# Kernel tuning notes

Measured on AMD Instinct MI355X. Metric: run time of the kernel, lower is better.

## Reference

```python
import jax, jax.numpy as jnp
import numpy as np
from jax import lax

V, E, H, S, B = 32000, 150, 30, 128, 32
STDV = 1.0 / np.sqrt(30.0)


def setup_inputs() -> dict:
    key = jax.random.key(0)
    ks = jax.random.split(key, 9)
    u = lambda k, shape: jax.random.uniform(k, shape, jnp.float32, -STDV, STDV)
    return {
        "input_batch": jax.random.randint(ks[0], (S, B), 0, V),
        "embedding": u(ks[1], (V, E)),
        "W_ih_lr": u(ks[2], (E + H, H)),
        "b_ih_lr": u(ks[3], (1, H)),
        "W_ih_rl": u(ks[4], (E + H, H)),
        "b_ih_rl": u(ks[5], (1, H)),
        "W_ho": u(ks[6], (2 * H, V)),
        "b_ho": u(ks[7], (1, V)),
        "initial_hidden": u(ks[8], (1, H)),
    }


def reference(input_batch, embedding, W_ih_lr, b_ih_lr, W_ih_rl, b_ih_rl,
              W_ho, b_ho, initial_hidden):
    seq_len, batch = input_batch.shape
    emb = embedding[input_batch]  # (S, B, E)
    # original code detaches the initial hidden state (uses .data)
    init = jnp.broadcast_to(lax.stop_gradient(initial_hidden), (batch, initial_hidden.shape[1]))

    def step(W, b):
        def f(h, w):
            h_new = jnp.tanh(jnp.concatenate([w, h], axis=1) @ W + b)
            return h_new, h_new
        return f

    # forward (left-to-right): f_states[t] = hLR[t+1]
    _, f_states = lax.scan(step(W_ih_lr, b_ih_lr), init, emb)
    # backward (right-to-left) over reversed tokens: r_states[k] = hRL[S-1-k]
    _, r_states = lax.scan(step(W_ih_rl, b_ih_rl), init, emb[::-1])

    # prediction at i uses hLR[i] and hRL[i+1]
    hLR_used = jnp.concatenate([init[None], f_states[:-1]], axis=0)        # hLR[0..S-1]
    hRL_used = jnp.concatenate([r_states[:-1][::-1], init[None]], axis=0)  # hRL[1..S]

    h_cat = jnp.concatenate([hLR_used, hRL_used], axis=-1)  # (S, B, 2H)
    logits = jnp.einsum('sbh,hv->sbv', h_cat, W_ho) + b_ho  # (S, B, V)
    return jax.nn.log_softmax(logits, axis=-1)
```

## Files before the change

kernel.cpp:

```cpp
#include <hip/hip_runtime.h>

#define VSZ 32000
#define ESZ 150
#define HSZ 30
#define SSZ 128
#define BSZ 32
#define SB  4096
#define KP  64

typedef __attribute__((ext_vector_type(8))) short bf16x8;
typedef __attribute__((ext_vector_type(4))) float f32x4;
typedef __attribute__((ext_vector_type(8))) unsigned short u16x8;

static __device__ __forceinline__ unsigned short f2bf(float f) {
  unsigned int u = __float_as_uint(f);
  u += 0x7fffu + ((u >> 16) & 1u);
  return (unsigned short)(u >> 16);
}

__global__ void k_zproj(const int* __restrict__ idx, const float* __restrict__ emb,
                        const float* __restrict__ Wlr, const float* __restrict__ blr,
                        const float* __restrict__ Wrl, const float* __restrict__ brl,
                        float* __restrict__ z) {
  __shared__ float erow[ESZ];
  int tb = blockIdx.x;
  int row = idx[tb];
  for (int i = threadIdx.x; i < ESZ; i += 64) erow[i] = emb[row * ESZ + i];
  __syncthreads();
  int lane = threadIdx.x;
  int j = lane & 31, dir = lane >> 5;
  if (j < HSZ) {
    const float* W = dir ? Wrl : Wlr;
    float acc = dir ? brl[j] : blr[j];
#pragma unroll 10
    for (int e = 0; e < ESZ; ++e) acc = fmaf(erow[e], W[e * HSZ + j], acc);
    z[(dir * SB + tb) * HSZ + j] = acc;
  }
}

__global__ void k_scan(const float* __restrict__ z, const float* __restrict__ Wlr,
                       const float* __restrict__ Wrl, const float* __restrict__ h0,
                       unsigned short* __restrict__ hcat) {
  int lane = threadIdx.x;
  int half = lane >> 5, j = lane & 31;
  int chain = blockIdx.x * 2 + half;
  int dir = chain >> 5, b = chain & 31;
  const float* W = dir ? Wrl : Wlr;
  float w2[HSZ];
#pragma unroll
  for (int k = 0; k < HSZ; ++k) w2[k] = (j < HSZ) ? W[(ESZ + k) * HSZ + j] : 0.f;
  float h = (j < HSZ) ? h0[j] : 0.f;
  int dim = (j < HSZ) ? dir * HSZ + j : (dir ? 60 : 62) + (j - 30);
  unsigned short padbits = (dim == 60) ? f2bf(1.0f) : (unsigned short)0;
  const float* zc = z + dir * (SB * HSZ) + b * HSZ + j;
  int src = half << 5;
  int te0 = dir ? (SSZ - 1) : 0;
  float zv = (j < HSZ) ? zc[te0 * (BSZ * HSZ)] : 0.f;
  for (int t = 0; t < SSZ; ++t) {
    int te = dir ? (SSZ - 1 - t) : t;
    float zn = 0.f;
    if (t < SSZ - 1) {
      int ten = dir ? (SSZ - 2 - t) : (t + 1);
      zn = (j < HSZ) ? zc[ten * (BSZ * HSZ)] : 0.f;
    }
    int r = te * BSZ + b;
    hcat[r * KP + dim] = (j < HSZ) ? f2bf(h) : padbits;
    float a0 = zv, a1 = 0.f, a2 = 0.f, a3 = 0.f;
#pragma unroll
    for (int k = 0; k < 28; k += 4) {
      a0 = fmaf(__shfl(h, src + k),     w2[k],     a0);
      a1 = fmaf(__shfl(h, src + k + 1), w2[k + 1], a1);
      a2 = fmaf(__shfl(h, src + k + 2), w2[k + 2], a2);
      a3 = fmaf(__shfl(h, src + k + 3), w2[k + 3], a3);
    }
    a0 = fmaf(__shfl(h, src + 28), w2[28], a0);
    a1 = fmaf(__shfl(h, src + 29), w2[29], a1);
    float x = (a0 + a1) + (a2 + a3);
    h = tanhf(x);
    zv = zn;
  }
}

__global__ void k_wprep(const float* __restrict__ Who, const float* __restrict__ bho,
                        unsigned short* __restrict__ Wbt) {
  int v = blockIdx.x * 256 + threadIdx.x;
  int kq = blockIdx.y;
  u16x8 pack;
#pragma unroll
  for (int i = 0; i < 8; ++i) {
    int k = kq * 8 + i;
    float val = (k < 60) ? Who[k * VSZ + v] : ((k == 60) ? bho[v] : 0.f);
    pack[i] = f2bf(val);
  }
  *(u16x8*)&Wbt[v * KP + kq * 8] = pack;
}

__global__ void k_sumexp(const unsigned short* __restrict__ hcat,
                         const unsigned short* __restrict__ Wbt,
                         float* __restrict__ part) {
  int mb = blockIdx.x, nb = blockIdx.y;
  int wave = threadIdx.x >> 6, lane = threadIdx.x & 63;
  int g = lane >> 4, c = lane & 15;
  int rbase = mb * 128 + wave * 32;
  bf16x8 a[2][2];
#pragma unroll
  for (int mt = 0; mt < 2; ++mt)
#pragma unroll
    for (int ks = 0; ks < 2; ++ks)
      a[mt][ks] = *(const bf16x8*)&hcat[(rbase + mt * 16 + c) * KP + ks * 32 + g * 8];
  float se[2][4] = {{0.f, 0.f, 0.f, 0.f}, {0.f, 0.f, 0.f, 0.f}};
  int c0 = nb * 2000;
  for (int nt = 0; nt < 125; ++nt) {
    int col = c0 + nt * 16 + c;
    bf16x8 b0 = *(const bf16x8*)&Wbt[col * KP + g * 8];
    bf16x8 b1 = *(const bf16x8*)&Wbt[col * KP + 32 + g * 8];
#pragma unroll
    for (int mt = 0; mt < 2; ++mt) {
      f32x4 acc = {0.f, 0.f, 0.f, 0.f};
      acc = __builtin_amdgcn_mfma_f32_16x16x32_bf16(a[mt][0], b0, acc, 0, 0, 0);
      acc = __builtin_amdgcn_mfma_f32_16x16x32_bf16(a[mt][1], b1, acc, 0, 0, 0);
#pragma unroll
      for (int i = 0; i < 4; ++i) se[mt][i] += __expf(acc[i]);
    }
  }
#pragma unroll
  for (int off = 1; off < 16; off <<= 1)
#pragma unroll
    for (int mt = 0; mt < 2; ++mt)
#pragma unroll
      for (int i = 0; i < 4; ++i) se[mt][i] += __shfl_xor(se[mt][i], off);
  if (c == 0) {
#pragma unroll
    for (int mt = 0; mt < 2; ++mt)
#pragma unroll
      for (int i = 0; i < 4; ++i)
        part[(rbase + mt * 16 + g * 4 + i) * 16 + nb] = se[mt][i];
  }
}

__global__ void k_writeout(const unsigned short* __restrict__ hcat,
                           const unsigned short* __restrict__ Wbt,
                           const float* __restrict__ part,
                           float* __restrict__ out) {
  __shared__ float Lsh[128];
  int mb = blockIdx.x, nb = blockIdx.y;
  int tid = threadIdx.x;
  if (tid < 128) {
    const float* p = &part[(mb * 128 + tid) * 16];
    float s = 0.f;
#pragma unroll
    for (int k = 0; k < 16; ++k) s += p[k];
    Lsh[tid] = logf(s);
  }
  __syncthreads();
  int wave = tid >> 6, lane = tid & 63;
  int g = lane >> 4, c = lane & 15;
  int rbase = mb * 128 + wave * 32;
  bf16x8 a[2][2];
#pragma unroll
  for (int mt = 0; mt < 2; ++mt)
#pragma unroll
    for (int ks = 0; ks < 2; ++ks)
      a[mt][ks] = *(const bf16x8*)&hcat[(rbase + mt * 16 + c) * KP + ks * 32 + g * 8];
  float L[2][4];
#pragma unroll
  for (int mt = 0; mt < 2; ++mt)
#pragma unroll
    for (int i = 0; i < 4; ++i)
      L[mt][i] = Lsh[wave * 32 + mt * 16 + g * 4 + i];
  int c0 = nb * 2000;
  for (int nt = 0; nt < 125; ++nt) {
    int col = c0 + nt * 16 + c;
    bf16x8 b0 = *(const bf16x8*)&Wbt[col * KP + g * 8];
    bf16x8 b1 = *(const bf16x8*)&Wbt[col * KP + 32 + g * 8];
#pragma unroll
    for (int mt = 0; mt < 2; ++mt) {
      f32x4 acc = {0.f, 0.f, 0.f, 0.f};
      acc = __builtin_amdgcn_mfma_f32_16x16x32_bf16(a[mt][0], b0, acc, 0, 0, 0);
      acc = __builtin_amdgcn_mfma_f32_16x16x32_bf16(a[mt][1], b1, acc, 0, 0, 0);
#pragma unroll
      for (int i = 0; i < 4; ++i)
        out[(rbase + mt * 16 + g * 4 + i) * VSZ + col] = acc[i] - L[mt][i];
    }
  }
}

extern "C" void kernel_launch(void* const* d_in, const int* in_sizes, int n_in,
                              void* d_out, int out_size, void* d_ws, size_t ws_size,
                              hipStream_t stream) {
  (void)in_sizes; (void)n_in; (void)out_size; (void)ws_size;
  const int*   idx = (const int*)d_in[0];
  const float* emb = (const float*)d_in[1];
  const float* Wlr = (const float*)d_in[2];
  const float* blr = (const float*)d_in[3];
  const float* Wrl = (const float*)d_in[4];
  const float* brl = (const float*)d_in[5];
  const float* Who = (const float*)d_in[6];
  const float* bho = (const float*)d_in[7];
  const float* h0  = (const float*)d_in[8];
  float* out = (float*)d_out;

  char* ws = (char*)d_ws;
  float*          z    = (float*)(ws + 0);
  unsigned short* hcat = (unsigned short*)(ws + 983040);
  unsigned short* Wbt  = (unsigned short*)(ws + 1507328);
  float*          part = (float*)(ws + 5603328);

  k_zproj<<<SB, 64, 0, stream>>>(idx, emb, Wlr, blr, Wrl, brl, z);
  k_wprep<<<dim3(125, 8), 256, 0, stream>>>(Who, bho, Wbt);
  k_scan<<<32, 64, 0, stream>>>(z, Wlr, Wrl, h0, hcat);
  k_sumexp<<<dim3(32, 16), 256, 0, stream>>>(hcat, Wbt, part);
  k_writeout<<<dim3(32, 16), 256, 0, stream>>>(hcat, Wbt, part, out);
}
```

Measured before the change: 321.1 us.

## Swap MFMA operands for row-contiguous vector stores, readlane scan, fast tanh

The output GEMMs now put the weight tile in the A operand and the hidden states in B. Each lane therefore holds four consecutive vocab columns of one row, so the log-softmax output can be written with 16-byte vector stores instead of scattered scalar stores, and the sum-exp reduction gets simpler. The recurrent scan now runs one chain per 64-lane block and broadcasts hidden values with readlane instead of shuffles. It also replaces tanhf with an exp-based formula, which may lose a little accuracy near zero. The launch order of the scan and the weight-prep kernel is swapped.

```diff
diff --git a/kernel.cpp b/kernel.cpp
--- a/kernel.cpp
+++ b/kernel.cpp
@@ -16,6 +16,10 @@
   unsigned int u = __float_as_uint(f);
   u += 0x7fffu + ((u >> 16) & 1u);
   return (unsigned short)(u >> 16);
+}
+
+static __device__ __forceinline__ float readlane_f(float v, int lane) {
+  return __uint_as_float(__builtin_amdgcn_readlane(__float_as_uint(v), lane));
 }
 
 __global__ void k_zproj(const int* __restrict__ idx, const float* __restrict__ emb,
@@ -41,19 +45,18 @@
 __global__ void k_scan(const float* __restrict__ z, const float* __restrict__ Wlr,
                        const float* __restrict__ Wrl, const float* __restrict__ h0,
                        unsigned short* __restrict__ hcat) {
-  int lane = threadIdx.x;
-  int half = lane >> 5, j = lane & 31;
-  int chain = blockIdx.x * 2 + half;
+  int j = threadIdx.x;
+  int chain = blockIdx.x;
   int dir = chain >> 5, b = chain & 31;
   const float* W = dir ? Wrl : Wlr;
   float w2[HSZ];
 #pragma unroll
   for (int k = 0; k < HSZ; ++k) w2[k] = (j < HSZ) ? W[(ESZ + k) * HSZ + j] : 0.f;
   float h = (j < HSZ) ? h0[j] : 0.f;
+  bool wr = (j < 32);
   int dim = (j < HSZ) ? dir * HSZ + j : (dir ? 60 : 62) + (j - 30);
   unsigned short padbits = (dim == 60) ? f2bf(1.0f) : (unsigned short)0;
   const float* zc = z + dir * (SB * HSZ) + b * HSZ + j;
-  int src = half << 5;
   int te0 = dir ? (SSZ - 1) : 0;
   float zv = (j < HSZ) ? zc[te0 * (BSZ * HSZ)] : 0.f;
   for (int t = 0; t < SSZ; ++t) {
@@ -64,19 +67,20 @@
       zn = (j < HSZ) ? zc[ten * (BSZ * HSZ)] : 0.f;
     }
     int r = te * BSZ + b;
-    hcat[r * KP + dim] = (j < HSZ) ? f2bf(h) : padbits;
+    if (wr) hcat[r * KP + dim] = (j < HSZ) ? f2bf(h) : padbits;
     float a0 = zv, a1 = 0.f, a2 = 0.f, a3 = 0.f;
 #pragma unroll
     for (int k = 0; k < 28; k += 4) {
-      a0 = fmaf(__shfl(h, src + k),     w2[k],     a0);
-      a1 = fmaf(__shfl(h, src + k + 1), w2[k + 1], a1);
-      a2 = fmaf(__shfl(h, src + k + 2), w2[k + 2], a2);
-      a3 = fmaf(__shfl(h, src + k + 3), w2[k + 3], a3);
-    }
-    a0 = fmaf(__shfl(h, src + 28), w2[28], a0);
-    a1 = fmaf(__shfl(h, src + 29), w2[29], a1);
+      a0 = fmaf(readlane_f(h, k),     w2[k],     a0);
+      a1 = fmaf(readlane_f(h, k + 1), w2[k + 1], a1);
+      a2 = fmaf(readlane_f(h, k + 2), w2[k + 2], a2);
+      a3 = fmaf(readlane_f(h, k + 3), w2[k + 3], a3);
+    }
+    a0 = fmaf(readlane_f(h, 28), w2[28], a0);
+    a1 = fmaf(readlane_f(h, 29), w2[29], a1);
     float x = (a0 + a1) + (a2 + a3);
-    h = tanhf(x);
+    float e = __expf(2.0f * x);
+    h = 1.0f - __fdividef(2.0f, e + 1.0f);
     zv = zn;
   }
 }
@@ -102,39 +106,35 @@
   int wave = threadIdx.x >> 6, lane = threadIdx.x & 63;
   int g = lane >> 4, c = lane & 15;
   int rbase = mb * 128 + wave * 32;
-  bf16x8 a[2][2];
-#pragma unroll
-  for (int mt = 0; mt < 2; ++mt)
+  bf16x8 bfr[2][2];
+#pragma unroll
+  for (int rg = 0; rg < 2; ++rg)
 #pragma unroll
     for (int ks = 0; ks < 2; ++ks)
-      a[mt][ks] = *(const bf16x8*)&hcat[(rbase + mt * 16 + c) * KP + ks * 32 + g * 8];
-  float se[2][4] = {{0.f, 0.f, 0.f, 0.f}, {0.f, 0.f, 0.f, 0.f}};
+      bfr[rg][ks] = *(const bf16x8*)&hcat[(rbase + rg * 16 + c) * KP + ks * 32 + g * 8];
+  float se[2] = {0.f, 0.f};
   int c0 = nb * 2000;
   for (int nt = 0; nt < 125; ++nt) {
-    int col = c0 + nt * 16 + c;
-    bf16x8 b0 = *(const bf16x8*)&Wbt[col * KP + g * 8];
-    bf16x8 b1 = *(const bf16x8*)&Wbt[col * KP + 32 + g * 8];
-#pragma unroll
-    for (int mt = 0; mt < 2; ++mt) {
+    int ct = c0 + nt * 16;
+    bf16x8 a0 = *(const bf16x8*)&Wbt[(ct + c) * KP + g * 8];
+    bf16x8 a1 = *(const bf16x8*)&Wbt[(ct + c) * KP + 32 + g * 8];
+#pragma unroll
+    for (int rg = 0; rg < 2; ++rg) {
       f32x4 acc = {0.f, 0.f, 0.f, 0.f};
-      acc = __builtin_amdgcn_mfma_f32_16x16x32_bf16(a[mt][0], b0, acc, 0, 0, 0);
-      acc = __builtin_amdgcn_mfma_f32_16x16x32_bf16(a[mt][1], b1, acc, 0, 0, 0);
-#pragma unroll
-      for (int i = 0; i < 4; ++i) se[mt][i] += __expf(acc[i]);
-    }
-  }
-#pragma unroll
-  for (int off = 1; off < 16; off <<= 1)
-#pragma unroll
-    for (int mt = 0; mt < 2; ++mt)
-#pragma unroll
-      for (int i = 0; i < 4; ++i) se[mt][i] += __shfl_xor(se[mt][i], off);
-  if (c == 0) {
-#pragma unroll
-    for (int mt = 0; mt < 2; ++mt)
-#pragma unroll
-      for (int i = 0; i < 4; ++i)
-        part[(rbase + mt * 16 + g * 4 + i) * 16 + nb] = se[mt][i];
+      acc = __builtin_amdgcn_mfma_f32_16x16x32_bf16(a0, bfr[rg][0], acc, 0, 0, 0);
+      acc = __builtin_amdgcn_mfma_f32_16x16x32_bf16(a1, bfr[rg][1], acc, 0, 0, 0);
+      se[rg] += (__expf(acc[0]) + __expf(acc[1])) + (__expf(acc[2]) + __expf(acc[3]));
+    }
+  }
+#pragma unroll
+  for (int rg = 0; rg < 2; ++rg) {
+    se[rg] += __shfl_xor(se[rg], 16);
+    se[rg] += __shfl_xor(se[rg], 32);
+  }
+  if (g == 0) {
+#pragma unroll
+    for (int rg = 0; rg < 2; ++rg)
+      part[(rbase + rg * 16 + c) * 16 + nb] = se[rg];
   }
 }
 
@@ -156,31 +156,29 @@
   int wave = tid >> 6, lane = tid & 63;
   int g = lane >> 4, c = lane & 15;
   int rbase = mb * 128 + wave * 32;
-  bf16x8 a[2][2];
-#pragma unroll
-  for (int mt = 0; mt < 2; ++mt)
+  bf16x8 bfr[2][2];
+#pragma unroll
+  for (int rg = 0; rg < 2; ++rg)
 #pragma unroll
     for (int ks = 0; ks < 2; ++ks)
-      a[mt][ks] = *(const bf16x8*)&hcat[(rbase + mt * 16 + c) * KP + ks * 32 + g * 8];
-  float L[2][4];
-#pragma unroll
-  for (int mt = 0; mt < 2; ++mt)
-#pragma unroll
-    for (int i = 0; i < 4; ++i)
-      L[mt][i] = Lsh[wave * 32 + mt * 16 + g * 4 + i];
+      bfr[rg][ks] = *(const bf16x8*)&hcat[(rbase + rg * 16 + c) * KP + ks * 32 + g * 8];
+  float L[2];
+#pragma unroll
+  for (int rg = 0; rg < 2; ++rg) L[rg] = Lsh[wave * 32 + rg * 16 + c];
   int c0 = nb * 2000;
   for (int nt = 0; nt < 125; ++nt) {
-    int col = c0 + nt * 16 + c;
-    bf16x8 b0 = *(const bf16x8*)&Wbt[col * KP + g * 8];
-    bf16x8 b1 = *(const bf16x8*)&Wbt[col * KP + 32 + g * 8];
-#pragma unroll
-    for (int mt = 0; mt < 2; ++mt) {
+    int ct = c0 + nt * 16;
+    bf16x8 a0 = *(const bf16x8*)&Wbt[(ct + c) * KP + g * 8];
+    bf16x8 a1 = *(const bf16x8*)&Wbt[(ct + c) * KP + 32 + g * 8];
+#pragma unroll
+    for (int rg = 0; rg < 2; ++rg) {
       f32x4 acc = {0.f, 0.f, 0.f, 0.f};
-      acc = __builtin_amdgcn_mfma_f32_16x16x32_bf16(a[mt][0], b0, acc, 0, 0, 0);
-      acc = __builtin_amdgcn_mfma_f32_16x16x32_bf16(a[mt][1], b1, acc, 0, 0, 0);
-#pragma unroll
-      for (int i = 0; i < 4; ++i)
-        out[(rbase + mt * 16 + g * 4 + i) * VSZ + col] = acc[i] - L[mt][i];
+      acc = __builtin_amdgcn_mfma_f32_16x16x32_bf16(a0, bfr[rg][0], acc, 0, 0, 0);
+      acc = __builtin_amdgcn_mfma_f32_16x16x32_bf16(a1, bfr[rg][1], acc, 0, 0, 0);
+      f32x4 v;
+#pragma unroll
+      for (int i = 0; i < 4; ++i) v[i] = acc[i] - L[rg];
+      *(f32x4*)&out[(rbase + rg * 16 + c) * VSZ + ct + g * 4] = v;
     }
   }
 }
@@ -207,8 +205,8 @@
   float*          part = (float*)(ws + 5603328);
 
   k_zproj<<<SB, 64, 0, stream>>>(idx, emb, Wlr, blr, Wrl, brl, z);
+  k_scan<<<64, 64, 0, stream>>>(z, Wlr, Wrl, h0, hcat);
   k_wprep<<<dim3(125, 8), 256, 0, stream>>>(Who, bho, Wbt);
-  k_scan<<<32, 64, 0, stream>>>(z, Wlr, Wrl, h0, hcat);
   k_sumexp<<<dim3(32, 16), 256, 0, stream>>>(hcat, Wbt, part);
   k_writeout<<<dim3(32, 16), 256, 0, stream>>>(hcat, Wbt, part, out);
 }
```

Measured after the change: 316.2 us. About the same (-1.5%).
